# Kernel optimization log

Measured on AMD Instinct MI355X. Metric: run time of the kernel, lower is better.

The kernel has to match this reference:

```python
import jax, jax.numpy as jnp
import numpy as np

N_NODES = 50000
N_EDGES = 800000
HID = 256
ATOM_F = 256
BOND_F = 128
BN_EPS = 1e-5


def setup_inputs() -> dict:
    key = jax.random.key(0)
    ks = jax.random.split(key, 8)
    x = jax.random.normal(ks[0], (N_NODES, ATOM_F), dtype=jnp.float32)
    w = jax.random.normal(ks[1], (N_EDGES, BOND_F), dtype=jnp.float32)
    dst = jax.random.randint(ks[2], (N_EDGES,), 0, N_NODES, dtype=jnp.int32)
    # Linear weights (PyTorch layout: [out, in]) scaled like kaiming-uniform-ish
    W_atom = jax.random.normal(ks[3], (HID, ATOM_F), dtype=jnp.float32) / np.sqrt(ATOM_F)
    b_atom = jax.random.normal(ks[4], (HID,), dtype=jnp.float32) * 0.01
    W_bond = jax.random.normal(ks[5], (HID, BOND_F), dtype=jnp.float32) / np.sqrt(BOND_F)
    b_bond = jax.random.normal(ks[6], (HID,), dtype=jnp.float32) * 0.01
    gamma = jnp.ones((HID,), dtype=jnp.float32)
    beta = jnp.zeros((HID,), dtype=jnp.float32)
    return {"x": x, "w": w, "dst": dst, "W_atom": W_atom, "b_atom": b_atom,
            "W_bond": W_bond, "b_bond": b_bond, "gamma": gamma, "beta": beta}


def reference(x, w, dst, W_atom, b_atom, W_bond, b_bond, gamma, beta):
    # Per-edge linear projection of bond features: [E, HID]
    h_edge = jnp.einsum('ef,hf->eh', w, W_bond) + b_bond
    # Scatter-sum messages into destination nodes: [N, HID]
    agg = jax.ops.segment_sum(h_edge, dst, num_segments=x.shape[0])
    # Node linear + add aggregated messages
    h = agg + jnp.einsum('nf,hf->nh', x, W_atom) + b_atom
    # ReLU then BatchNorm1d (training mode: biased batch stats, affine)
    h = jax.nn.relu(h)
    mean = jnp.mean(h, axis=0)
    var = jnp.mean(jnp.square(h - mean), axis=0)
    out = (h - mean) * jax.lax.rsqrt(var + BN_EPS) * gamma + beta
    return out
```

## Files before the change

kernel.cpp:

```cpp
#include <hip/hip_runtime.h>

#define NN 50000
#define NE 800000
#define HIDN 256
#define AF 256
#define BF 128
#define KT 384
#define NCH64 782
#define GG 256
#define MAXDEG 128

typedef __attribute__((ext_vector_type(8))) short short8;
typedef __attribute__((ext_vector_type(4))) float f32x4;
typedef __attribute__((ext_vector_type(2))) float f32x2;

__device__ __forceinline__ unsigned short f2bf(float f) {
    union { float f; unsigned int u; } c; c.f = f;
    unsigned int u = c.u;
    return (unsigned short)((u + 0x7FFFu + ((u >> 16) & 1u)) >> 16);
}
__device__ __forceinline__ float bf2f(unsigned short u) {
    union { unsigned int u; float f; } c; c.u = (unsigned int)u << 16;
    return c.f;
}

__global__ __launch_bounds__(256) void k_sortW(const int4* __restrict__ dst4,
        int* __restrict__ cursor, int* __restrict__ sortedEdge,
        const float* __restrict__ Wa, const float* __restrict__ Wb,
        unsigned short* __restrict__ Wc) {
    const int i = blockIdx.x * 256 + threadIdx.x;
    if (i < NE / 4) {
        const int4 d = dst4[i];
        const int e = i * 4;
        int p;
        p = atomicAdd(cursor + d.x, 1); if (p < MAXDEG) sortedEdge[d.x * MAXDEG + p] = e;
        p = atomicAdd(cursor + d.y, 1); if (p < MAXDEG) sortedEdge[d.y * MAXDEG + p] = e + 1;
        p = atomicAdd(cursor + d.z, 1); if (p < MAXDEG) sortedEdge[d.z * MAXDEG + p] = e + 2;
        p = atomicAdd(cursor + d.w, 1); if (p < MAXDEG) sortedEdge[d.w * MAXDEG + p] = e + 3;
    }
    if (blockIdx.x < 48) {
        const int gid = blockIdx.x * 256 + threadIdx.x;
        const int j = gid / 48, cb = gid % 48;
        const float* src = (cb < 32) ? (Wa + j * AF + cb * 8) : (Wb + j * BF + (cb - 32) * 8);
        f32x4 a = reinterpret_cast<const f32x4*>(src)[0];
        f32x4 b = reinterpret_cast<const f32x4*>(src)[1];
        short8 s;
        s[0] = f2bf(a[0]); s[1] = f2bf(a[1]); s[2] = f2bf(a[2]); s[3] = f2bf(a[3]);
        s[4] = f2bf(b[0]); s[5] = f2bf(b[1]); s[6] = f2bf(b[2]); s[7] = f2bf(b[3]);
        *reinterpret_cast<short8*>(Wc + j * KT + cb * 8) = s;
    }
}

__global__ __launch_bounds__(256) void k_gather(const float* __restrict__ w,
        const int* __restrict__ sortedEdge, const int* __restrict__ cursor,
        unsigned short* __restrict__ agg) {
    const int node = blockIdx.x * 4 + (threadIdx.x >> 6);
    const int lane = threadIdx.x & 63;
    if (node >= NN) return;
    const int start = node * MAXDEG;
    const int degn = min(cursor[node], MAXDEG);
    const f32x2* __restrict__ w2 = reinterpret_cast<const f32x2*>(w);
    float ax = 0.f, ay = 0.f;
    for (int base = 0; base < degn; base += 64) {
        const int m = min(64, degn - base);
        int eid = 0;
        if (lane < m) eid = sortedEdge[start + base + lane];
        int i = 0;
        for (; i + 8 <= m; i += 8) {
            int e0 = __shfl(eid, i + 0), e1 = __shfl(eid, i + 1);
            int e2 = __shfl(eid, i + 2), e3 = __shfl(eid, i + 3);
            int e4 = __shfl(eid, i + 4), e5 = __shfl(eid, i + 5);
            int e6 = __shfl(eid, i + 6), e7 = __shfl(eid, i + 7);
            f32x2 v0 = __builtin_nontemporal_load(&w2[(size_t)e0 * 64 + lane]);
            f32x2 v1 = __builtin_nontemporal_load(&w2[(size_t)e1 * 64 + lane]);
            f32x2 v2 = __builtin_nontemporal_load(&w2[(size_t)e2 * 64 + lane]);
            f32x2 v3 = __builtin_nontemporal_load(&w2[(size_t)e3 * 64 + lane]);
            f32x2 v4 = __builtin_nontemporal_load(&w2[(size_t)e4 * 64 + lane]);
            f32x2 v5 = __builtin_nontemporal_load(&w2[(size_t)e5 * 64 + lane]);
            f32x2 v6 = __builtin_nontemporal_load(&w2[(size_t)e6 * 64 + lane]);
            f32x2 v7 = __builtin_nontemporal_load(&w2[(size_t)e7 * 64 + lane]);
            ax += ((v0.x + v1.x) + (v2.x + v3.x)) + ((v4.x + v5.x) + (v6.x + v7.x));
            ay += ((v0.y + v1.y) + (v2.y + v3.y)) + ((v4.y + v5.y) + (v6.y + v7.y));
        }
        for (; i < m; ++i) {
            int e = __shfl(eid, i);
            f32x2 v = __builtin_nontemporal_load(&w2[(size_t)e * 64 + lane]);
            ax += v.x;
            ay += v.y;
        }
    }
    unsigned int pack = (unsigned int)f2bf(ax) | ((unsigned int)f2bf(ay) << 16);
    *reinterpret_cast<unsigned int*>(agg + (size_t)node * BF + lane * 2) = pack;
}

#define LOADCH(ch) do { \
    const int base_ = (ch) * 64; \
    const int g0_ = base_ + xr0; \
    if (g0_ < NN) { const f32x4* s_ = reinterpret_cast<const f32x4*>(x + (size_t)g0_ * AF + xkb * 8); \
        xa0 = __builtin_nontemporal_load(s_); xb0 = __builtin_nontemporal_load(s_ + 1); } \
    else { xa0 = f32x4{0.f,0.f,0.f,0.f}; xb0 = f32x4{0.f,0.f,0.f,0.f}; } \
    if (g0_ + 16 < NN) { const f32x4* s_ = reinterpret_cast<const f32x4*>(x + (size_t)(g0_ + 16) * AF + xkb * 8); \
        xa1 = __builtin_nontemporal_load(s_); xb1 = __builtin_nontemporal_load(s_ + 1); } \
    else { xa1 = f32x4{0.f,0.f,0.f,0.f}; xb1 = f32x4{0.f,0.f,0.f,0.f}; } \
    if (g0_ + 32 < NN) { const f32x4* s_ = reinterpret_cast<const f32x4*>(x + (size_t)(g0_ + 32) * AF + xkb * 8); \
        xa2 = __builtin_nontemporal_load(s_); xb2 = __builtin_nontemporal_load(s_ + 1); } \
    else { xa2 = f32x4{0.f,0.f,0.f,0.f}; xb2 = f32x4{0.f,0.f,0.f,0.f}; } \
    if (g0_ + 48 < NN) { const f32x4* s_ = reinterpret_cast<const f32x4*>(x + (size_t)(g0_ + 48) * AF + xkb * 8); \
        xa3 = __builtin_nontemporal_load(s_); xb3 = __builtin_nontemporal_load(s_ + 1); } \
    else { xa3 = f32x4{0.f,0.f,0.f,0.f}; xb3 = f32x4{0.f,0.f,0.f,0.f}; } \
    const int g2_ = base_ + gr_; \
    if (g2_ < NN) { ga0 = *reinterpret_cast<const short8*>(agg + (size_t)g2_ * BF + gkb * 8); } \
    else { ga0 = short8{0,0,0,0,0,0,0,0}; } \
    if (g2_ + 32 < NN) { ga1 = *reinterpret_cast<const short8*>(agg + (size_t)(g2_ + 32) * BF + gkb * 8); } \
    else { ga1 = short8{0,0,0,0,0,0,0,0}; } \
} while (0)

#define WRROW(XA, XB, ROW) do { \
    short8 s_; \
    s_[0]=f2bf(XA[0]); s_[1]=f2bf(XA[1]); s_[2]=f2bf(XA[2]); s_[3]=f2bf(XA[3]); \
    s_[4]=f2bf(XB[0]); s_[5]=f2bf(XB[1]); s_[6]=f2bf(XB[2]); s_[7]=f2bf(XB[3]); \
    *reinterpret_cast<short8*>(BUF + (ROW) * KT + ((xkb ^ ((ROW) & 7)) << 3)) = s_; \
} while (0)

#define WRITECH(B_) do { \
    unsigned short* BUF = (B_); \
    WRROW(xa0, xb0, xr0); \
    WRROW(xa1, xb1, xr0 + 16); \
    WRROW(xa2, xb2, xr0 + 32); \
    WRROW(xa3, xb3, xr0 + 48); \
    *reinterpret_cast<short8*>(BUF + gr_ * KT + (((32 + gkb) ^ (gr_ & 7)) << 3)) = ga0; \
    *reinterpret_cast<short8*>(BUF + (gr_ + 32) * KT + (((32 + gkb) ^ ((gr_ + 32) & 7)) << 3)) = ga1; \
} while (0)

__global__ __launch_bounds__(512, 1) void k_gemm(const float* __restrict__ x,
        const unsigned short* __restrict__ agg, const int* __restrict__ cnt,
        const unsigned short* __restrict__ Wc, const float* __restrict__ b_atom,
        const float* __restrict__ b_bond, unsigned short* __restrict__ hbf,
        float* __restrict__ colsum, float* __restrict__ colsumsq) {
    __shared__ unsigned short As0[64 * KT];
    __shared__ unsigned short As1[64 * KT];

    const int tid = threadIdx.x;
    const int wid = tid >> 6, lane = tid & 63;
    const int lrow = lane & 15, lk = lane >> 4;
    const int colb = wid * 32;

    short8 breg[2][12];
    #pragma unroll
    for (int t = 0; t < 2; ++t)
        #pragma unroll
        for (int kt = 0; kt < 12; ++kt)
            breg[t][kt] = *reinterpret_cast<const short8*>(
                Wc + (size_t)(colb + t * 16 + lrow) * KT + kt * 32 + lk * 8);

    const float ba0 = b_atom[colb + lrow],      bb0 = b_bond[colb + lrow];
    const float ba1 = b_atom[colb + 16 + lrow], bb1 = b_bond[colb + 16 + lrow];

    f32x4 xa0, xb0, xa1, xb1, xa2, xb2, xa3, xb3;
    short8 ga0, ga1;
    const int xr0 = tid >> 5, xkb = tid & 31;
    const int gr_ = tid >> 4, gkb = tid & 15;

    float st0 = 0.f, st20 = 0.f, st1 = 0.f, st21 = 0.f;

    auto compute = [&](int chunk, const unsigned short* A) {
        f32x4 acc[4][2];
        #pragma unroll
        for (int rt = 0; rt < 4; ++rt) {
            acc[rt][0] = f32x4{0.f,0.f,0.f,0.f};
            acc[rt][1] = f32x4{0.f,0.f,0.f,0.f};
        }
        #pragma unroll
        for (int kt = 0; kt < 12; ++kt) {
            const int kb = kt * 4 + lk;
            const int so = (kb ^ (lrow & 7)) << 3;
            #pragma unroll
            for (int rt = 0; rt < 4; ++rt) {
                short8 f = *reinterpret_cast<const short8*>(
                    A + (rt * 16 + lrow) * KT + so);
                acc[rt][0] = __builtin_amdgcn_mfma_f32_16x16x32_bf16(f, breg[0][kt], acc[rt][0], 0, 0, 0);
                acc[rt][1] = __builtin_amdgcn_mfma_f32_16x16x32_bf16(f, breg[1][kt], acc[rt][1], 0, 0, 0);
            }
        }
        #pragma unroll
        for (int rt = 0; rt < 4; ++rt) {
            const int row0 = chunk * 64 + rt * 16 + lk * 4;
            #pragma unroll
            for (int r2 = 0; r2 < 4; ++r2) {
                const int gr = row0 + r2;
                if (gr < NN) {
                    const float dg = (float)cnt[gr];
                    const float v0 = fmaxf(acc[rt][0][r2] + ba0 + dg * bb0, 0.f);
                    const float v1 = fmaxf(acc[rt][1][r2] + ba1 + dg * bb1, 0.f);
                    hbf[(size_t)gr * HIDN + colb + lrow]      = f2bf(v0);
                    hbf[(size_t)gr * HIDN + colb + 16 + lrow] = f2bf(v1);
                    st0 += v0; st20 += v0 * v0;
                    st1 += v1; st21 += v1 * v1;
                }
            }
        }
    };

    LOADCH(blockIdx.x);
    WRITECH(As0);
    asm volatile("s_waitcnt lgkmcnt(0)" ::: "memory");
    __builtin_amdgcn_s_barrier();

    int chunk = blockIdx.x;
    int buf = 0;
    while (true) {
        const bool more = (chunk + GG < NCH64);
        if (more) LOADCH(chunk + GG);
        compute(chunk, buf ? As1 : As0);
        if (!more) break;
        WRITECH(buf ? As0 : As1);
        asm volatile("s_waitcnt lgkmcnt(0)" ::: "memory");
        __builtin_amdgcn_s_barrier();
        chunk += GG;
        buf ^= 1;
    }

    st0 += __shfl_xor(st0, 16); st0 += __shfl_xor(st0, 32);
    st20 += __shfl_xor(st20, 16); st20 += __shfl_xor(st20, 32);
    st1 += __shfl_xor(st1, 16); st1 += __shfl_xor(st1, 32);
    st21 += __shfl_xor(st21, 16); st21 += __shfl_xor(st21, 32);
    if (lane < 16) {
        atomicAdd(colsum + colb + lane, st0);
        atomicAdd(colsumsq + colb + lane, st20);
        atomicAdd(colsum + colb + 16 + lane, st1);
        atomicAdd(colsumsq + colb + 16 + lane, st21);
    }
}

__global__ __launch_bounds__(256) void k_bn(const unsigned short* __restrict__ hbf,
        const float* __restrict__ colsum, const float* __restrict__ colsumsq,
        const float* __restrict__ gamma, const float* __restrict__ beta,
        float* __restrict__ out) {
    __shared__ float scs[HIDN], shs[HIDN];
    const int t = threadIdx.x;
    {
        const float mean = colsum[t] * (1.f / NN);
        const float var = colsumsq[t] * (1.f / NN) - mean * mean;
        const float sc = gamma[t] * rsqrtf(var + 1e-5f);
        scs[t] = sc;
        shs[t] = beta[t] - mean * sc;
    }
    __syncthreads();
    const int total = NN * HIDN / 8;
    const short8* __restrict__ h8 = reinterpret_cast<const short8*>(hbf);
    f32x4* __restrict__ out4 = reinterpret_cast<f32x4*>(out);
    for (int gid = blockIdx.x * 256 + t; gid < total; gid += gridDim.x * 256) {
        const short8 v = __builtin_nontemporal_load(&h8[gid]);
        const int c = (gid & 31) * 8;
        f32x4 r0, r1;
        #pragma unroll
        for (int k = 0; k < 4; ++k)
            r0[k] = fmaf(bf2f((unsigned short)v[k]), scs[c + k], shs[c + k]);
        #pragma unroll
        for (int k = 0; k < 4; ++k)
            r1[k] = fmaf(bf2f((unsigned short)v[4 + k]), scs[c + 4 + k], shs[c + 4 + k]);
        __builtin_nontemporal_store(r0, &out4[gid * 2]);
        __builtin_nontemporal_store(r1, &out4[gid * 2 + 1]);
    }
}

extern "C" void kernel_launch(void* const* d_in, const int* in_sizes, int n_in,
                              void* d_out, int out_size, void* d_ws, size_t ws_size,
                              hipStream_t stream) {
    const float* x      = (const float*)d_in[0];
    const float* w      = (const float*)d_in[1];
    const int*   dst    = (const int*)d_in[2];
    const float* W_atom = (const float*)d_in[3];
    const float* b_atom = (const float*)d_in[4];
    const float* W_bond = (const float*)d_in[5];
    const float* b_bond = (const float*)d_in[6];
    const float* gamma  = (const float*)d_in[7];
    const float* beta   = (const float*)d_in[8];
    float* out = (float*)d_out;

    int*   cursor     = (int*)d_ws;
    float* colsum     = (float*)(cursor + NN);
    float* colsumsq   = colsum + HIDN;
    int*   sortedEdge = (int*)(colsumsq + HIDN);
    unsigned short* Wc  = (unsigned short*)(sortedEdge + (size_t)NN * MAXDEG);
    unsigned short* agg = Wc + (size_t)HIDN * KT;
    unsigned short* hbf = agg + (size_t)NN * BF;

    hipMemsetAsync(d_ws, 0, (size_t)(NN + 2 * HIDN) * 4, stream);

    k_sortW<<<(NE / 4 + 255) / 256, 256, 0, stream>>>((const int4*)dst, cursor,
                                                      sortedEdge, W_atom, W_bond, Wc);
    k_gather<<<(NN + 3) / 4, 256, 0, stream>>>(w, sortedEdge, cursor, agg);
    k_gemm<<<GG, 512, 0, stream>>>(x, agg, cursor, Wc, b_atom, b_bond,
                                   hbf, colsum, colsumsq);
    k_bn<<<2048, 256, 0, stream>>>(hbf, colsum, colsumsq, gamma, beta, out);
}
```

Baseline: 194.8 us.

## Pre-convert x to bf16 in sort kernel and simplify GEMM tile staging

The fp32 node features are now converted to bf16 inside the first (sort/weight-convert) kernel and written to a workspace buffer. The GEMM then loads pre-converted bf16 rows for both x and agg with one uniform 6-iteration staging loop, swizzling on the global side. This moves conversion work off the GEMM's load path, hides it behind the atomic-bound sort kernel, and halves the GEMM's read bytes for x. In exchange it adds an extra fp32 read plus a bf16 write and reread of x (about 25 MB of extra traffic), and the staging loop has integer division.

```diff
diff --git a/kernel.cpp b/kernel.cpp
--- a/kernel.cpp
+++ b/kernel.cpp
@@ -27,7 +27,8 @@
 __global__ __launch_bounds__(256) void k_sortW(const int4* __restrict__ dst4,
         int* __restrict__ cursor, int* __restrict__ sortedEdge,
         const float* __restrict__ Wa, const float* __restrict__ Wb,
-        unsigned short* __restrict__ Wc) {
+        unsigned short* __restrict__ Wc, const float* __restrict__ x,
+        unsigned short* __restrict__ xbf) {
     const int i = blockIdx.x * 256 + threadIdx.x;
     if (i < NE / 4) {
         const int4 d = dst4[i];
@@ -48,6 +49,16 @@
         s[0] = f2bf(a[0]); s[1] = f2bf(a[1]); s[2] = f2bf(a[2]); s[3] = f2bf(a[3]);
         s[4] = f2bf(b[0]); s[5] = f2bf(b[1]); s[6] = f2bf(b[2]); s[7] = f2bf(b[3]);
         *reinterpret_cast<short8*>(Wc + j * KT + cb * 8) = s;
+    }
+    const int nthr = gridDim.x * 256;
+    for (int t = i; t < NN * AF / 8; t += nthr) {
+        const f32x4* s = reinterpret_cast<const f32x4*>(x + (size_t)t * 8);
+        f32x4 a = __builtin_nontemporal_load(s);
+        f32x4 b = __builtin_nontemporal_load(s + 1);
+        short8 v;
+        v[0] = f2bf(a[0]); v[1] = f2bf(a[1]); v[2] = f2bf(a[2]); v[3] = f2bf(a[3]);
+        v[4] = f2bf(b[0]); v[5] = f2bf(b[1]); v[6] = f2bf(b[2]); v[7] = f2bf(b[3]);
+        *reinterpret_cast<short8*>(xbf + (size_t)t * 8) = v;
     }
 }
 
@@ -94,45 +105,34 @@
 }
 
 #define LOADCH(ch) do { \
-    const int base_ = (ch) * 64; \
-    const int g0_ = base_ + xr0; \
-    if (g0_ < NN) { const f32x4* s_ = reinterpret_cast<const f32x4*>(x + (size_t)g0_ * AF + xkb * 8); \
-        xa0 = __builtin_nontemporal_load(s_); xb0 = __builtin_nontemporal_load(s_ + 1); } \
-    else { xa0 = f32x4{0.f,0.f,0.f,0.f}; xb0 = f32x4{0.f,0.f,0.f,0.f}; } \
-    if (g0_ + 16 < NN) { const f32x4* s_ = reinterpret_cast<const f32x4*>(x + (size_t)(g0_ + 16) * AF + xkb * 8); \
-        xa1 = __builtin_nontemporal_load(s_); xb1 = __builtin_nontemporal_load(s_ + 1); } \
-    else { xa1 = f32x4{0.f,0.f,0.f,0.f}; xb1 = f32x4{0.f,0.f,0.f,0.f}; } \
-    if (g0_ + 32 < NN) { const f32x4* s_ = reinterpret_cast<const f32x4*>(x + (size_t)(g0_ + 32) * AF + xkb * 8); \
-        xa2 = __builtin_nontemporal_load(s_); xb2 = __builtin_nontemporal_load(s_ + 1); } \
-    else { xa2 = f32x4{0.f,0.f,0.f,0.f}; xb2 = f32x4{0.f,0.f,0.f,0.f}; } \
-    if (g0_ + 48 < NN) { const f32x4* s_ = reinterpret_cast<const f32x4*>(x + (size_t)(g0_ + 48) * AF + xkb * 8); \
-        xa3 = __builtin_nontemporal_load(s_); xb3 = __builtin_nontemporal_load(s_ + 1); } \
-    else { xa3 = f32x4{0.f,0.f,0.f,0.f}; xb3 = f32x4{0.f,0.f,0.f,0.f}; } \
-    const int g2_ = base_ + gr_; \
-    if (g2_ < NN) { ga0 = *reinterpret_cast<const short8*>(agg + (size_t)g2_ * BF + gkb * 8); } \
-    else { ga0 = short8{0,0,0,0,0,0,0,0}; } \
-    if (g2_ + 32 < NN) { ga1 = *reinterpret_cast<const short8*>(agg + (size_t)(g2_ + 32) * BF + gkb * 8); } \
-    else { ga1 = short8{0,0,0,0,0,0,0,0}; } \
-} while (0)
-
-#define WRROW(XA, XB, ROW) do { \
-    short8 s_; \
-    s_[0]=f2bf(XA[0]); s_[1]=f2bf(XA[1]); s_[2]=f2bf(XA[2]); s_[3]=f2bf(XA[3]); \
-    s_[4]=f2bf(XB[0]); s_[5]=f2bf(XB[1]); s_[6]=f2bf(XB[2]); s_[7]=f2bf(XB[3]); \
-    *reinterpret_cast<short8*>(BUF + (ROW) * KT + ((xkb ^ ((ROW) & 7)) << 3)) = s_; \
+    const int rowbase_ = (ch) * 64; \
+    _Pragma("unroll") \
+    for (int it_ = 0; it_ < 6; ++it_) { \
+        const int s_ = it_ * 512 + tid; \
+        const int r_ = s_ / 48, c_ = s_ - r_ * 48; \
+        const int cg_ = c_ ^ (r_ & 7); \
+        const int grow_ = rowbase_ + r_; \
+        short8 v_ = short8{0,0,0,0,0,0,0,0}; \
+        if (grow_ < NN) { \
+            v_ = (cg_ < 32) \
+               ? *reinterpret_cast<const short8*>(xbf + (size_t)grow_ * AF + cg_ * 8) \
+               : *reinterpret_cast<const short8*>(agg + (size_t)grow_ * BF + (cg_ - 32) * 8); \
+        } \
+        stg[it_] = v_; \
+    } \
 } while (0)
 
 #define WRITECH(B_) do { \
     unsigned short* BUF = (B_); \
-    WRROW(xa0, xb0, xr0); \
-    WRROW(xa1, xb1, xr0 + 16); \
-    WRROW(xa2, xb2, xr0 + 32); \
-    WRROW(xa3, xb3, xr0 + 48); \
-    *reinterpret_cast<short8*>(BUF + gr_ * KT + (((32 + gkb) ^ (gr_ & 7)) << 3)) = ga0; \
-    *reinterpret_cast<short8*>(BUF + (gr_ + 32) * KT + (((32 + gkb) ^ ((gr_ + 32) & 7)) << 3)) = ga1; \
+    _Pragma("unroll") \
+    for (int it_ = 0; it_ < 6; ++it_) { \
+        const int s_ = it_ * 512 + tid; \
+        const int r_ = s_ / 48, c_ = s_ - r_ * 48; \
+        *reinterpret_cast<short8*>(BUF + r_ * KT + c_ * 8) = stg[it_]; \
+    } \
 } while (0)
 
-__global__ __launch_bounds__(512, 1) void k_gemm(const float* __restrict__ x,
+__global__ __launch_bounds__(512, 1) void k_gemm(const unsigned short* __restrict__ xbf,
         const unsigned short* __restrict__ agg, const int* __restrict__ cnt,
         const unsigned short* __restrict__ Wc, const float* __restrict__ b_atom,
         const float* __restrict__ b_bond, unsigned short* __restrict__ hbf,
@@ -156,11 +156,7 @@
     const float ba0 = b_atom[colb + lrow],      bb0 = b_bond[colb + lrow];
     const float ba1 = b_atom[colb + 16 + lrow], bb1 = b_bond[colb + 16 + lrow];
 
-    f32x4 xa0, xb0, xa1, xb1, xa2, xb2, xa3, xb3;
-    short8 ga0, ga1;
-    const int xr0 = tid >> 5, xkb = tid & 31;
-    const int gr_ = tid >> 4, gkb = tid & 15;
-
+    short8 stg[6];
     float st0 = 0.f, st20 = 0.f, st1 = 0.f, st21 = 0.f;
 
     auto compute = [&](int chunk, const unsigned short* A) {
@@ -284,14 +280,16 @@
     int*   sortedEdge = (int*)(colsumsq + HIDN);
     unsigned short* Wc  = (unsigned short*)(sortedEdge + (size_t)NN * MAXDEG);
     unsigned short* agg = Wc + (size_t)HIDN * KT;
-    unsigned short* hbf = agg + (size_t)NN * BF;
+    unsigned short* xbf = agg + (size_t)NN * BF;
+    unsigned short* hbf = xbf + (size_t)NN * AF;
 
     hipMemsetAsync(d_ws, 0, (size_t)(NN + 2 * HIDN) * 4, stream);
 
     k_sortW<<<(NE / 4 + 255) / 256, 256, 0, stream>>>((const int4*)dst, cursor,
-                                                      sortedEdge, W_atom, W_bond, Wc);
+                                                      sortedEdge, W_atom, W_bond, Wc,
+                                                      x, xbf);
     k_gather<<<(NN + 3) / 4, 256, 0, stream>>>(w, sortedEdge, cursor, agg);
-    k_gemm<<<GG, 512, 0, stream>>>(x, agg, cursor, Wc, b_atom, b_bond,
+    k_gemm<<<GG, 512, 0, stream>>>(xbf, agg, cursor, Wc, b_atom, b_bond,
                                    hbf, colsum, colsumsq);
     k_bn<<<2048, 256, 0, stream>>>(hbf, colsum, colsumsq, gamma, beta, out);
 }
```

Measured after the change: 207.4 us. +6.4%, slower.
